# Kernel optimization log

Measured on AMD Instinct MI355X. Metric: run time of the kernel, lower is better.

The kernel has to match this reference:

```python
import jax, jax.numpy as jnp
import numpy as np

B, S, HID = 2, 2048, 2048
NH, NKV, DH = 32, 8, 64
WIN = 1024


def rotate_half(x):
    x1, x2 = x[..., : x.shape[-1] // 2], x[..., x.shape[-1] // 2:]
    return jnp.concatenate((-x2, x1), axis=-1)


def setup_inputs() -> dict:
    key = jax.random.key(0)
    ks = jax.random.split(key, 8)
    hidden_states = jax.random.normal(ks[0], (B, S, HID), dtype=jnp.float32)
    # real RoPE tables: [B, S, DH]
    inv_freq = 1.0 / (10000.0 ** (np.arange(0, DH, 2, dtype=np.float32) / DH))
    ang = np.arange(S, dtype=np.float32)[:, None] * inv_freq[None, :]  # [S, DH/2]
    emb = np.concatenate([ang, ang], axis=-1)  # [S, DH]
    cos = jnp.broadcast_to(jnp.asarray(np.cos(emb)), (B, S, DH))
    sin = jnp.broadcast_to(jnp.asarray(np.sin(emb)), (B, S, DH))
    sc = 0.02
    Wq = jax.random.normal(ks[1], (NH * DH, HID), dtype=jnp.float32) * sc
    Wk = jax.random.normal(ks[2], (NKV * DH, HID), dtype=jnp.float32) * sc
    Wv = jax.random.normal(ks[3], (NKV * DH, HID), dtype=jnp.float32) * sc
    Wo = jax.random.normal(ks[4], (HID, NH * DH), dtype=jnp.float32) * sc
    return {"hidden_states": hidden_states, "cos": cos, "sin": sin,
            "Wq": Wq, "Wk": Wk, "Wv": Wv, "Wo": Wo}


def sliding_window_mask(q_len, k_len, dtype):
    half = WIN // 2
    qi = jnp.arange(q_len)[:, None]
    ki = jnp.arange(k_len)[None, :]
    last = jnp.clip(qi + half, None, k_len - 1)
    first = jnp.clip(qi - half, 0, None)
    visible = (ki >= first) & (ki <= last)
    minv = jnp.finfo(dtype).min
    return jnp.where(visible, jnp.array(0.0, dtype), jnp.array(minv, dtype))  # [q_len, k_len]


def reference(hidden_states, cos, sin, Wq, Wk, Wv, Wo):
    b, s, _ = hidden_states.shape
    scale = DH ** -0.5
    q = (hidden_states @ Wq.T).reshape(b, s, NH, DH).transpose(0, 2, 1, 3)   # [B,NH,S,DH]
    k = (hidden_states @ Wk.T).reshape(b, s, NKV, DH).transpose(0, 2, 1, 3)  # [B,NKV,S,DH]
    v = (hidden_states @ Wv.T).reshape(b, s, NKV, DH).transpose(0, 2, 1, 3)
    c, sn = cos[:, None, :, :], sin[:, None, :, :]  # broadcast over heads
    q = q * c + rotate_half(q) * sn
    k = k * c + rotate_half(k) * sn
    groups = NH // NKV
    k = jnp.repeat(k, groups, axis=1)  # [B,NH,S,DH]
    v = jnp.repeat(v, groups, axis=1)
    mask = sliding_window_mask(s, s, hidden_states.dtype)  # [S,S]
    scores = jnp.einsum("bhqd,bhkd->bhqk", q, k) * scale + mask  # dense quadratic bias add
    attn = jax.nn.softmax(scores, axis=-1)
    out = jnp.einsum("bhqk,bhkd->bhqd", attn, v)
    out = out.transpose(0, 2, 1, 3).reshape(b, s, NH * DH)
    return out @ Wo.T
```

## Files before the change

kernel.cpp:

```cpp
#include <hip/hip_runtime.h>
#include <hip/hip_bf16.h>
#include <stdint.h>
#include <stddef.h>

#define S_LEN 2048
#define HIDDEN 2048
#define NHEAD 32
#define NKVH 8
#define DHEAD 64
#define BATCH 2
#define HALFW 512
#define QSCALE 0.18033688011112042f

typedef __attribute__((ext_vector_type(4))) float f32x4;
typedef __attribute__((ext_vector_type(8))) short short8;
typedef __attribute__((ext_vector_type(4))) short short4v;

__device__ __forceinline__ unsigned short f2bf(float f) {
  unsigned u = __builtin_bit_cast(unsigned, f);
  u += 0x7fffu + ((u >> 16) & 1u);
  return (unsigned short)(u >> 16);
}
__device__ __forceinline__ float bf2f(unsigned short h) {
  unsigned u = ((unsigned)h) << 16;
  return __builtin_bit_cast(float, u);
}

__global__ void k_cvt(const float* __restrict__ src, unsigned short* __restrict__ dst, int n4) {
  int i = blockIdx.x * blockDim.x + threadIdx.x;
  int stride = gridDim.x * blockDim.x;
  for (; i < n4; i += stride) {
    float4 v = reinterpret_cast<const float4*>(src)[i];
    short4v o;
    o[0] = (short)f2bf(v.x);
    o[1] = (short)f2bf(v.y);
    o[2] = (short)f2bf(v.z);
    o[3] = (short)f2bf(v.w);
    reinterpret_cast<short4v*>(dst)[i] = o;
  }
}

template <int CSTORE_F32>
__global__ __launch_bounds__(256) void k_gemm_bt(const unsigned short* __restrict__ A,
                                                 const unsigned short* __restrict__ Bw,
                                                 void* __restrict__ Cout,
                                                 int M, int N, int K) {
  __shared__ unsigned short As[128][32];
  __shared__ unsigned short Bs[128][32];
  const int tid = threadIdx.x;
  const int wid = tid >> 6;
  const int lane = tid & 63;
  const int l15 = lane & 15;
  const int lhi = lane >> 4;
  const int bm = blockIdx.y * 128;
  const int bn = blockIdx.x * 128;
  const int wm = (wid >> 1) * 64;
  const int wn = (wid & 1) * 64;
  f32x4 acc[4][4] = {};

  for (int k0 = 0; k0 < K; k0 += 32) {
#pragma unroll
    for (int i = 0; i < 2; ++i) {
      int u = i * 256 + tid;
      int row = u >> 2, c8 = u & 3;
      const unsigned short* ga = A + (size_t)(bm + row) * K + k0 + c8 * 8;
      const unsigned short* gb = Bw + (size_t)(bn + row) * K + k0 + c8 * 8;
      __builtin_amdgcn_global_load_lds(
          (const __attribute__((address_space(1))) unsigned int*)(const void*)ga,
          (__attribute__((address_space(3))) unsigned int*)(void*)((char*)&As[0][0] + i * 4096 + wid * 1024),
          16, 0, 0);
      __builtin_amdgcn_global_load_lds(
          (const __attribute__((address_space(1))) unsigned int*)(const void*)gb,
          (__attribute__((address_space(3))) unsigned int*)(void*)((char*)&Bs[0][0] + i * 4096 + wid * 1024),
          16, 0, 0);
    }
    __syncthreads();

    short8 af[4], bfr[4];
#pragma unroll
    for (int m = 0; m < 4; ++m)
      af[m] = *reinterpret_cast<const short8*>(&As[wm + m * 16 + l15][lhi * 8]);
#pragma unroll
    for (int n = 0; n < 4; ++n)
      bfr[n] = *reinterpret_cast<const short8*>(&Bs[wn + n * 16 + l15][lhi * 8]);
#pragma unroll
    for (int m = 0; m < 4; ++m)
#pragma unroll
      for (int n = 0; n < 4; ++n)
        acc[m][n] = __builtin_amdgcn_mfma_f32_16x16x32_bf16(af[m], bfr[n], acc[m][n], 0, 0, 0);
    __syncthreads();
  }

#pragma unroll
  for (int m = 0; m < 4; ++m) {
#pragma unroll
    for (int r = 0; r < 4; ++r) {
      int row = bm + wm + m * 16 + lhi * 4 + r;
#pragma unroll
      for (int n = 0; n < 4; ++n) {
        int col = bn + wn + n * 16 + l15;
        float v = acc[m][n][r];
        if (CSTORE_F32)
          ((float*)Cout)[(size_t)row * N + col] = v;
        else
          ((unsigned short*)Cout)[(size_t)row * N + col] = f2bf(v);
      }
    }
  }
}

__global__ void k_rope(const unsigned short* __restrict__ qkv,
                       const float* __restrict__ cosb, const float* __restrict__ sinb,
                       unsigned short* __restrict__ Qr, unsigned short* __restrict__ Kr) {
  int idx = blockIdx.x * blockDim.x + threadIdx.x;
  if (idx >= BATCH * S_LEN * 40 * 32) return;
  int d = idx & 31;
  int hh = (idx >> 5) % 40;
  int bs = idx / (40 * 32);
  int s = bs % S_LEN, b = bs / S_LEN;
  int row = b * S_LEN + s;
  float c = cosb[row * DHEAD + d];
  float sn = sinb[row * DHEAD + d];
  int col = (hh < 32) ? (hh * DHEAD + d) : (2048 + (hh - 32) * DHEAD + d);
  const unsigned short* p = qkv + (size_t)row * 3072;
  float x1 = bf2f(p[col]);
  float x2 = bf2f(p[col + 32]);
  float o1 = x1 * c - x2 * sn;
  float o2 = x2 * c + x1 * sn;
  if (hh < 32) {
    size_t o = ((size_t)(b * NHEAD + hh) * S_LEN + s) * DHEAD + d;
    Qr[o] = f2bf(o1 * QSCALE);
    Qr[o + 32] = f2bf(o2 * QSCALE);
  } else {
    size_t o = ((size_t)(b * NKVH + (hh - 32)) * S_LEN + s) * DHEAD + d;
    Kr[o] = f2bf(o1);
    Kr[o + 32] = f2bf(o2);
  }
}

__global__ void k_vt(const unsigned short* __restrict__ qkv, unsigned short* __restrict__ Vt) {
  __shared__ unsigned short t[64][68];
  int s0 = blockIdx.x * 64;
  int b = blockIdx.y >> 3, hk = blockIdx.y & 7;
  int tid = threadIdx.x;
#pragma unroll
  for (int it = 0; it < 4; ++it) {
    int u = it * 256 + tid;
    int srow = u >> 4, c4 = u & 15;
    short4v v = *reinterpret_cast<const short4v*>(
        &qkv[(size_t)(b * S_LEN + s0 + srow) * 3072 + 2560 + hk * 64 + c4 * 4]);
    *reinterpret_cast<short4v*>(&t[srow][c4 * 4]) = v;
  }
  __syncthreads();
#pragma unroll
  for (int it = 0; it < 4; ++it) {
    int u = it * 256 + tid;
    int d = u >> 4, s4 = u & 15;
    short4v v;
#pragma unroll
    for (int j = 0; j < 4; ++j) v[j] = t[s4 * 4 + j][d];
    *reinterpret_cast<short4v*>(
        &Vt[((size_t)(b * NKVH + hk) * DHEAD + d) * S_LEN + s0 + s4 * 4]) = v;
  }
}

__global__ __launch_bounds__(256) void k_attn(const unsigned short* __restrict__ Qr,
                                              const unsigned short* __restrict__ Kr,
                                              const unsigned short* __restrict__ Vt,
                                              unsigned short* __restrict__ AO) {
  __shared__ unsigned short Ks[2][64][64];
  __shared__ unsigned short Vs[2][64][64];
  __shared__ unsigned short Pl[4][16][72];

  const int tid = threadIdx.x, w = tid >> 6, lane = tid & 63;
  const int l15 = lane & 15, lhi = lane >> 4;

  int p = blockIdx.x;
  int L = (p & 7) * 256 + (p >> 3);
  int g = L >> 7;
  int b = g >> 3, hk = g & 7;
  int r_ = L & 127;
  int h = hk * 4 + (r_ >> 5);
  int q0b = (r_ & 31) * 64;
  const int qw = q0b + w * 16;

  const unsigned short* Qh = Qr + (size_t)(b * NHEAD + h) * S_LEN * DHEAD;
  const unsigned short* Kh = Kr + (size_t)(b * NKVH + hk) * S_LEN * DHEAD;
  const unsigned short* Vh = Vt + (size_t)(b * NKVH + hk) * DHEAD * S_LEN;

  short8 qf[2];
#pragma unroll
  for (int c = 0; c < 2; ++c)
    qf[c] = *reinterpret_cast<const short8*>(&Qh[(size_t)(qw + l15) * DHEAD + c * 32 + lhi * 8]);

  f32x4 o[4] = {};
  float den[4] = {0.f, 0.f, 0.f, 0.f};

  int klo = q0b - HALFW; if (klo < 0) klo = 0;
  klo &= ~63;
  int khi = q0b + 63 + HALFW; if (khi > S_LEN - 1) khi = S_LEN - 1;
  const int nt = ((khi + 1 - klo) + 63) >> 6;

  auto stage = [&](int bufidx, int kbb) {
#pragma unroll
    for (int i = 0; i < 2; ++i) {
      int u = i * 256 + tid;
      int row = u >> 3, c16 = u & 7;
      int sc = c16 ^ (row & 7);
      __builtin_amdgcn_global_load_lds(
          (const __attribute__((address_space(1))) unsigned int*)(const void*)
              (Kh + (size_t)(kbb + row) * DHEAD + sc * 8),
          (__attribute__((address_space(3))) unsigned int*)(void*)
              ((char*)&Ks[bufidx][0][0] + u * 16),
          16, 0, 0);
      __builtin_amdgcn_global_load_lds(
          (const __attribute__((address_space(1))) unsigned int*)(const void*)
              (Vh + (size_t)row * S_LEN + kbb + sc * 8),
          (__attribute__((address_space(3))) unsigned int*)(void*)
              ((char*)&Vs[bufidx][0][0] + u * 16),
          16, 0, 0);
    }
  };

  int cur = 0;
  stage(0, klo);
  __syncthreads();

  for (int t = 0; t < nt; ++t) {
    const int kb = klo + t * 64;
    if (t + 1 < nt) stage(cur ^ 1, kb + 64);

    f32x4 sacc[4] = {};
#pragma unroll
    for (int hh = 0; hh < 4; ++hh) {
      int kr = hh * 16 + l15;
      const char* kbase = (const char*)&Ks[cur][0][0] + kr * 128;
      short8 kf0 = *reinterpret_cast<const short8*>(kbase + ((lhi ^ (kr & 7)) * 16));
      short8 kf1 = *reinterpret_cast<const short8*>(kbase + (((4 + lhi) ^ (kr & 7)) * 16));
      sacc[hh] = __builtin_amdgcn_mfma_f32_16x16x32_bf16(qf[0], kf0, sacc[hh], 0, 0, 0);
      sacc[hh] = __builtin_amdgcn_mfma_f32_16x16x32_bf16(qf[1], kf1, sacc[hh], 0, 0, 0);
    }

    const bool inter = (kb >= qw + 15 - HALFW) && (kb + 63 <= qw + HALFW);
    if (inter) {
#pragma unroll
      for (int hh = 0; hh < 4; ++hh)
#pragma unroll
        for (int r = 0; r < 4; ++r) {
          float pv = __builtin_amdgcn_exp2f(sacc[hh][r]);
          unsigned short pb = f2bf(pv);
          Pl[w][lhi * 4 + r][hh * 16 + l15] = pb;
          den[r] += bf2f(pb);
        }
    } else {
#pragma unroll
      for (int hh = 0; hh < 4; ++hh)
#pragma unroll
        for (int r = 0; r < 4; ++r) {
          int q = qw + lhi * 4 + r;
          int key = kb + hh * 16 + l15;
          bool vis = (key >= q - HALFW) && (key <= q + HALFW);
          float pv = vis ? __builtin_amdgcn_exp2f(sacc[hh][r]) : 0.0f;
          unsigned short pb = f2bf(pv);
          Pl[w][lhi * 4 + r][hh * 16 + l15] = pb;
          den[r] += bf2f(pb);
        }
    }
    asm volatile("s_waitcnt lgkmcnt(0)" ::: "memory");

    short8 pf0 = *reinterpret_cast<const short8*>(&Pl[w][l15][lhi * 8]);
    short8 pf1 = *reinterpret_cast<const short8*>(&Pl[w][l15][32 + lhi * 8]);
#pragma unroll
    for (int c = 0; c < 4; ++c) {
      int d = c * 16 + l15;
      const char* vbase = (const char*)&Vs[cur][0][0] + d * 128;
      short8 vf0 = *reinterpret_cast<const short8*>(vbase + ((lhi ^ (d & 7)) * 16));
      short8 vf1 = *reinterpret_cast<const short8*>(vbase + (((4 + lhi) ^ (d & 7)) * 16));
      o[c] = __builtin_amdgcn_mfma_f32_16x16x32_bf16(pf0, vf0, o[c], 0, 0, 0);
      o[c] = __builtin_amdgcn_mfma_f32_16x16x32_bf16(pf1, vf1, o[c], 0, 0, 0);
    }

    __syncthreads();
    cur ^= 1;
  }

#pragma unroll
  for (int r = 0; r < 4; ++r) {
    float d = den[r];
    d += __shfl_xor(d, 1);
    d += __shfl_xor(d, 2);
    d += __shfl_xor(d, 4);
    d += __shfl_xor(d, 8);
    den[r] = d;
  }

#pragma unroll
  for (int r = 0; r < 4; ++r) {
    int q = qw + lhi * 4 + r;
    float dinv = 1.0f / den[r];
#pragma unroll
    for (int c = 0; c < 4; ++c)
      AO[(size_t)(b * S_LEN + q) * HIDDEN + h * DHEAD + c * 16 + l15] = f2bf(o[c][r] * dinv);
  }
}

extern "C" void kernel_launch(void* const* d_in, const int* in_sizes, int n_in,
                              void* d_out, int out_size, void* d_ws, size_t ws_size,
                              hipStream_t stream) {
  const float* hs   = (const float*)d_in[0];
  const float* cosb = (const float*)d_in[1];
  const float* sinb = (const float*)d_in[2];
  const float* Wq   = (const float*)d_in[3];
  const float* Wk   = (const float*)d_in[4];
  const float* Wv   = (const float*)d_in[5];
  const float* Wo   = (const float*)d_in[6];

  char* ws = (char*)d_ws;
  unsigned short* Xbf  = (unsigned short*)(ws);
  unsigned short* Wqkv = (unsigned short*)(ws + 16777216);
  unsigned short* QKV  = (unsigned short*)(ws + 16777216 + 12582912);
  unsigned short* Wob  = (unsigned short*)(ws + 16777216 + 12582912 + 25165824);

  unsigned short* Qr = Xbf;
  unsigned short* Kr = Wqkv;
  unsigned short* Vt = (unsigned short*)(ws + 16777216 + 4194304);
  unsigned short* AO = QKV;

  {
    int n4 = 8388608 / 4;
    k_cvt<<<4096, 256, 0, stream>>>(hs, Xbf, n4);
  }
  k_cvt<<<4096, 256, 0, stream>>>(Wq, Wqkv, 4194304 / 4);
  k_cvt<<<1024, 256, 0, stream>>>(Wk, Wqkv + 4194304, 1048576 / 4);
  k_cvt<<<1024, 256, 0, stream>>>(Wv, Wqkv + 5242880, 1048576 / 4);
  k_cvt<<<4096, 256, 0, stream>>>(Wo, Wob, 4194304 / 4);

  k_gemm_bt<0><<<dim3(3072 / 128, 4096 / 128), 256, 0, stream>>>(Xbf, Wqkv, (void*)QKV, 4096, 3072, 2048);

  k_rope<<<(BATCH * S_LEN * 40 * 32) / 256, 256, 0, stream>>>(QKV, cosb, sinb, Qr, Kr);
  k_vt<<<dim3(S_LEN / 64, BATCH * NKVH), 256, 0, stream>>>(QKV, Vt);

  k_attn<<<BATCH * NHEAD * (S_LEN / 64), 256, 0, stream>>>(Qr, Kr, Vt, AO);

  k_gemm_bt<1><<<dim3(2048 / 128, 4096 / 128), 256, 0, stream>>>(AO, Wob, d_out, 4096, 2048, 2048);
}
```

Baseline: 235.9 us.

## Fuse conversion kernels and transpose score MFMA for packed P stores

Merges the five fp32-to-bf16 conversion launches into one kernel that dispatches on the index range, removing four launch gaps. In attention, the QK^T MFMA operands are swapped so each lane holds four consecutive keys of one query. This lets P be written with packed v_cvt_pk_bf16 stores into a swizzled LDS buffer and the row sum be kept in a single scalar per lane. It also sets launch_bounds occupancy to 4 and shrinks the P padding. The denominator now sums unrounded fp32 probabilities instead of bf16-rounded ones, which changes numerics slightly.

```diff
diff --git a/kernel.cpp b/kernel.cpp
--- a/kernel.cpp
+++ b/kernel.cpp
@@ -15,6 +15,7 @@
 typedef __attribute__((ext_vector_type(4))) float f32x4;
 typedef __attribute__((ext_vector_type(8))) short short8;
 typedef __attribute__((ext_vector_type(4))) short short4v;
+typedef __attribute__((ext_vector_type(2))) unsigned int u32x2;
 
 __device__ __forceinline__ unsigned short f2bf(float f) {
   unsigned u = __builtin_bit_cast(unsigned, f);
@@ -25,18 +26,37 @@
   unsigned u = ((unsigned)h) << 16;
   return __builtin_bit_cast(float, u);
 }
-
-__global__ void k_cvt(const float* __restrict__ src, unsigned short* __restrict__ dst, int n4) {
+__device__ __forceinline__ unsigned cvt_pk_bf16(float lo, float hi) {
+  unsigned r;
+  asm("v_cvt_pk_bf16_f32 %0, %1, %2" : "=v"(r) : "v"(lo), "v"(hi));
+  return r;
+}
+
+__global__ void k_cvt5(const float* __restrict__ s0, const float* __restrict__ s1,
+                       const float* __restrict__ s2, const float* __restrict__ s3,
+                       const float* __restrict__ s4,
+                       unsigned short* __restrict__ d0, unsigned short* __restrict__ d1,
+                       unsigned short* __restrict__ d2, unsigned short* __restrict__ d3,
+                       unsigned short* __restrict__ d4) {
   int i = blockIdx.x * blockDim.x + threadIdx.x;
-  int stride = gridDim.x * blockDim.x;
-  for (; i < n4; i += stride) {
-    float4 v = reinterpret_cast<const float4*>(src)[i];
+#pragma unroll 1
+  for (int it = 0; it < 9; ++it, i += 524288) {
+    const float* src;
+    unsigned short* dst;
+    int base;
+    if (i < 2097152)      { src = s0; dst = d0; base = 0; }
+    else if (i < 3145728) { src = s1; dst = d1; base = 2097152; }
+    else if (i < 3407872) { src = s2; dst = d2; base = 3145728; }
+    else if (i < 3670016) { src = s3; dst = d3; base = 3407872; }
+    else                  { src = s4; dst = d4; base = 3670016; }
+    int j = i - base;
+    float4 v = reinterpret_cast<const float4*>(src)[j];
     short4v o;
     o[0] = (short)f2bf(v.x);
     o[1] = (short)f2bf(v.y);
     o[2] = (short)f2bf(v.z);
     o[3] = (short)f2bf(v.w);
-    reinterpret_cast<short4v*>(dst)[i] = o;
+    reinterpret_cast<short4v*>(dst)[j] = o;
   }
 }
 
@@ -164,13 +184,13 @@
   }
 }
 
-__global__ __launch_bounds__(256) void k_attn(const unsigned short* __restrict__ Qr,
-                                              const unsigned short* __restrict__ Kr,
-                                              const unsigned short* __restrict__ Vt,
-                                              unsigned short* __restrict__ AO) {
+__global__ __launch_bounds__(256, 4) void k_attn(const unsigned short* __restrict__ Qr,
+                                                 const unsigned short* __restrict__ Kr,
+                                                 const unsigned short* __restrict__ Vt,
+                                                 unsigned short* __restrict__ AO) {
   __shared__ unsigned short Ks[2][64][64];
   __shared__ unsigned short Vs[2][64][64];
-  __shared__ unsigned short Pl[4][16][72];
+  __shared__ unsigned short Pl[4][16][64];
 
   const int tid = threadIdx.x, w = tid >> 6, lane = tid & 63;
   const int l15 = lane & 15, lhi = lane >> 4;
@@ -194,7 +214,12 @@
     qf[c] = *reinterpret_cast<const short8*>(&Qh[(size_t)(qw + l15) * DHEAD + c * 32 + lhi * 8]);
 
   f32x4 o[4] = {};
-  float den[4] = {0.f, 0.f, 0.f, 0.f};
+  float den = 0.f;
+  const int q = qw + l15;
+  const int kvisLo = q - HALFW, kvisHi = q + HALFW;
+
+  char* plbase = (char*)&Pl[w][0][0];
+  const int swz = (l15 & 7) << 4;
 
   int klo = q0b - HALFW; if (klo < 0) klo = 0;
   klo &= ~63;
@@ -237,39 +262,46 @@
       const char* kbase = (const char*)&Ks[cur][0][0] + kr * 128;
       short8 kf0 = *reinterpret_cast<const short8*>(kbase + ((lhi ^ (kr & 7)) * 16));
       short8 kf1 = *reinterpret_cast<const short8*>(kbase + (((4 + lhi) ^ (kr & 7)) * 16));
-      sacc[hh] = __builtin_amdgcn_mfma_f32_16x16x32_bf16(qf[0], kf0, sacc[hh], 0, 0, 0);
-      sacc[hh] = __builtin_amdgcn_mfma_f32_16x16x32_bf16(qf[1], kf1, sacc[hh], 0, 0, 0);
+      sacc[hh] = __builtin_amdgcn_mfma_f32_16x16x32_bf16(kf0, qf[0], sacc[hh], 0, 0, 0);
+      sacc[hh] = __builtin_amdgcn_mfma_f32_16x16x32_bf16(kf1, qf[1], sacc[hh], 0, 0, 0);
     }
 
     const bool inter = (kb >= qw + 15 - HALFW) && (kb + 63 <= qw + HALFW);
     if (inter) {
 #pragma unroll
-      for (int hh = 0; hh < 4; ++hh)
+      for (int hh = 0; hh < 4; ++hh) {
+        float p0 = __builtin_amdgcn_exp2f(sacc[hh][0]);
+        float p1 = __builtin_amdgcn_exp2f(sacc[hh][1]);
+        float p2 = __builtin_amdgcn_exp2f(sacc[hh][2]);
+        float p3 = __builtin_amdgcn_exp2f(sacc[hh][3]);
+        den += (p0 + p1) + (p2 + p3);
+        u32x2 pw;
+        pw[0] = cvt_pk_bf16(p0, p1);
+        pw[1] = cvt_pk_bf16(p2, p3);
+        *(u32x2*)(plbase + ((l15 * 128 + hh * 32 + lhi * 8) ^ swz)) = pw;
+      }
+    } else {
+#pragma unroll
+      for (int hh = 0; hh < 4; ++hh) {
+        float pp[4];
 #pragma unroll
         for (int r = 0; r < 4; ++r) {
-          float pv = __builtin_amdgcn_exp2f(sacc[hh][r]);
-          unsigned short pb = f2bf(pv);
-          Pl[w][lhi * 4 + r][hh * 16 + l15] = pb;
-          den[r] += bf2f(pb);
+          int key = kb + hh * 16 + lhi * 4 + r;
+          bool vis = (key >= kvisLo) && (key <= kvisHi);
+          pp[r] = vis ? __builtin_amdgcn_exp2f(sacc[hh][r]) : 0.0f;
         }
-    } else {
-#pragma unroll
-      for (int hh = 0; hh < 4; ++hh)
-#pragma unroll
-        for (int r = 0; r < 4; ++r) {
-          int q = qw + lhi * 4 + r;
-          int key = kb + hh * 16 + l15;
-          bool vis = (key >= q - HALFW) && (key <= q + HALFW);
-          float pv = vis ? __builtin_amdgcn_exp2f(sacc[hh][r]) : 0.0f;
-          unsigned short pb = f2bf(pv);
-          Pl[w][lhi * 4 + r][hh * 16 + l15] = pb;
-          den[r] += bf2f(pb);
-        }
+        den += (pp[0] + pp[1]) + (pp[2] + pp[3]);
+        u32x2 pw;
+        pw[0] = cvt_pk_bf16(pp[0], pp[1]);
+        pw[1] = cvt_pk_bf16(pp[2], pp[3]);
+        *(u32x2*)(plbase + ((l15 * 128 + hh * 32 + lhi * 8) ^ swz)) = pw;
+      }
     }
     asm volatile("s_waitcnt lgkmcnt(0)" ::: "memory");
-
-    short8 pf0 = *reinterpret_cast<const short8*>(&Pl[w][l15][lhi * 8]);
-    short8 pf1 = *reinterpret_cast<const short8*>(&Pl[w][l15][32 + lhi * 8]);
+    __builtin_amdgcn_sched_barrier(0);
+
+    short8 pf0 = *reinterpret_cast<const short8*>(plbase + ((l15 * 128 + lhi * 16) ^ swz));
+    short8 pf1 = *reinterpret_cast<const short8*>(plbase + ((l15 * 128 + 64 + lhi * 16) ^ swz));
 #pragma unroll
     for (int c = 0; c < 4; ++c) {
       int d = c * 16 + l15;
@@ -284,23 +316,17 @@
     cur ^= 1;
   }
 
+  den += __shfl_xor(den, 16);
+  den += __shfl_xor(den, 32);
+
 #pragma unroll
   for (int r = 0; r < 4; ++r) {
-    float d = den[r];
-    d += __shfl_xor(d, 1);
-    d += __shfl_xor(d, 2);
-    d += __shfl_xor(d, 4);
-    d += __shfl_xor(d, 8);
-    den[r] = d;
-  }
-
-#pragma unroll
-  for (int r = 0; r < 4; ++r) {
-    int q = qw + lhi * 4 + r;
-    float dinv = 1.0f / den[r];
+    int qo = qw + lhi * 4 + r;
+    float dr = __shfl(den, lhi * 4 + r, 64);
+    float dinv = 1.0f / dr;
 #pragma unroll
     for (int c = 0; c < 4; ++c)
-      AO[(size_t)(b * S_LEN + q) * HIDDEN + h * DHEAD + c * 16 + l15] = f2bf(o[c][r] * dinv);
+      AO[(size_t)(b * S_LEN + qo) * HIDDEN + h * DHEAD + c * 16 + l15] = f2bf(o[c][r] * dinv);
   }
 }
 
@@ -326,14 +352,8 @@
   unsigned short* Vt = (unsigned short*)(ws + 16777216 + 4194304);
   unsigned short* AO = QKV;
 
-  {
-    int n4 = 8388608 / 4;
-    k_cvt<<<4096, 256, 0, stream>>>(hs, Xbf, n4);
-  }
-  k_cvt<<<4096, 256, 0, stream>>>(Wq, Wqkv, 4194304 / 4);
-  k_cvt<<<1024, 256, 0, stream>>>(Wk, Wqkv + 4194304, 1048576 / 4);
-  k_cvt<<<1024, 256, 0, stream>>>(Wv, Wqkv + 5242880, 1048576 / 4);
-  k_cvt<<<4096, 256, 0, stream>>>(Wo, Wob, 4194304 / 4);
+  k_cvt5<<<2048, 256, 0, stream>>>(hs, Wq, Wk, Wv, Wo,
+                                   Xbf, Wqkv, Wqkv + 4194304, Wqkv + 5242880, Wob);
 
   k_gemm_bt<0><<<dim3(3072 / 128, 4096 / 128), 256, 0, stream>>>(Xbf, Wqkv, (void*)QKV, 4096, 3072, 2048);
 
```

Measured after the change: 216.7 us. -8.1%, faster.
